# Kernel tuning notes

Measured on AMD Instinct MI355X. Metric: run time of the kernel, lower is better.

Reference implementation:

```python
import jax, jax.numpy as jnp
import numpy as np

D = 1024      # hidden_dim
E = 8         # num_experts
F = 512       # expert_dim


def setup_inputs() -> dict:
    key = jax.random.key(0)
    ks = jax.random.split(key, 7)
    B, N = 4, 4096
    s1 = 1.0 / np.sqrt(D)
    s2 = 1.0 / np.sqrt(F)
    return {
        "x": jax.random.normal(ks[0], (B, N, D), dtype=jnp.float32),
        "W1": jax.random.uniform(ks[1], (E, D, F), jnp.float32, -s1, s1),  # per-expert first linear
        "b1": jax.random.uniform(ks[2], (E, F), jnp.float32, -s1, s1),
        "W2": jax.random.uniform(ks[3], (E, F, D), jnp.float32, -s2, s2),  # per-expert second linear
        "b2": jax.random.uniform(ks[4], (E, D), jnp.float32, -s2, s2),
        "Wr": jax.random.uniform(ks[5], (D, E), jnp.float32, -s1, s1),    # router
        "br": jax.random.uniform(ks[6], (E,), jnp.float32, -s1, s1),
    }


def reference(x, W1, b1, W2, b2, Wr, br):
    # Router: softmax over experts per token. [B,N,E]
    router_weights = jax.nn.softmax(x @ Wr + br, axis=-1)
    # All experts on all tokens (dense soft-MoE), batched as grouped GEMMs.
    h = jax.nn.gelu(jnp.einsum('bnd,edf->bnef', x, W1) + b1, approximate=False)  # [B,N,E,F]
    y = jnp.einsum('bnef,efd->bned', h, W2) + b2[None, None]                      # [B,N,E,D]
    # Softmax-weighted combine over experts.
    return jnp.einsum('bned,bne->bnd', y, router_weights)
```

## Files before the change

kernel.cpp:

```cpp
#include <hip/hip_runtime.h>
#include <hip/hip_bf16.h>
#include <math.h>

#define MTOK 16384
#define DDIM 1024
#define EEXP 8
#define FDIM 512
#define EFK  4096

typedef __attribute__((ext_vector_type(8))) short short8;
typedef __attribute__((ext_vector_type(4))) float floatx4;

__device__ __forceinline__ void gld_lds16(const void* g, void* l) {
  __builtin_amdgcn_global_load_lds((const __attribute__((address_space(1))) void*)g,
                                   (__attribute__((address_space(3))) void*)l, 16, 0, 0);
}

__device__ __forceinline__ float gelu_fast(float v) {
  const float z  = v * 0.70710678118654752f;
  const float az = fabsf(z);
  const float t  = __builtin_amdgcn_rcpf(1.f + 0.3275911f * az);
  const float poly = t * (0.254829592f +
                     t * (-0.284496736f +
                     t * (1.421413741f +
                     t * (-1.453152027f +
                     t * 1.061405429f))));
  const float ex = __expf(-az * az);
  float erfv = 1.f - poly * ex;
  erfv = copysignf(erfv, z);
  return 0.5f * v * (1.f + erfv);
}

__global__ __launch_bounds__(256) void transpose_cast_kernel(
    const float* __restrict__ in, __hip_bfloat16* __restrict__ out, int R, int C) {
  __shared__ float tile[32][33];
  const float* inb = in + (size_t)blockIdx.z * R * C;
  __hip_bfloat16* outb = out + (size_t)blockIdx.z * R * C;
  const int c0 = blockIdx.x * 32, r0 = blockIdx.y * 32;
  const int tx = threadIdx.x & 31, ty = threadIdx.x >> 5;
#pragma unroll
  for (int i = 0; i < 4; ++i)
    tile[ty + i * 8][tx] = inb[(size_t)(r0 + ty + i * 8) * C + (c0 + tx)];
  __syncthreads();
#pragma unroll
  for (int i = 0; i < 4; ++i)
    outb[(size_t)(c0 + ty + i * 8) * R + (r0 + tx)] = __float2bfloat16(tile[tx][ty + i * 8]);
}

__global__ __launch_bounds__(256) void router_cast_kernel(
    const float* __restrict__ x, const float* __restrict__ Wr, const float* __restrict__ br,
    __hip_bfloat16* __restrict__ xbf, float* __restrict__ r) {
  const int wave = (blockIdx.x * 256 + threadIdx.x) >> 6;
  const int lane = threadIdx.x & 63;
  const float* xr = x + (size_t)wave * DDIM;
  float acc[EEXP];
#pragma unroll
  for (int e = 0; e < EEXP; ++e) acc[e] = 0.f;
#pragma unroll
  for (int i = 0; i < DDIM / 64; ++i) {
    const int d = i * 64 + lane;
    const float xv = xr[d];
    xbf[(size_t)wave * DDIM + d] = __float2bfloat16(xv);
    const float4* w4 = (const float4*)(Wr + (size_t)d * EEXP);
    const float4 w0 = w4[0], w1 = w4[1];
    acc[0] += xv * w0.x; acc[1] += xv * w0.y; acc[2] += xv * w0.z; acc[3] += xv * w0.w;
    acc[4] += xv * w1.x; acc[5] += xv * w1.y; acc[6] += xv * w1.z; acc[7] += xv * w1.w;
  }
#pragma unroll
  for (int off = 32; off; off >>= 1) {
#pragma unroll
    for (int e = 0; e < EEXP; ++e) acc[e] += __shfl_xor(acc[e], off, 64);
  }
  float mx = -1e30f;
#pragma unroll
  for (int e = 0; e < EEXP; ++e) { acc[e] += br[e]; mx = fmaxf(mx, acc[e]); }
  float s = 0.f;
#pragma unroll
  for (int e = 0; e < EEXP; ++e) { acc[e] = expf(acc[e] - mx); s += acc[e]; }
  const float inv = 1.f / s;
  if (lane < EEXP) r[(size_t)wave * EEXP + lane] = acc[lane] * inv;
}

#define BUFB  24576
#define BOFFB 8192

#define STAGE3(O2, K0)                                                          \
  do {                                                                          \
    gld_lds16(pA  + (K0), ldsb + (O2) + (tid << 4));                            \
    gld_lds16(pB0 + (K0), ldsb + (O2) + 8192  + (tid << 4));                    \
    gld_lds16(pB1 + (K0), ldsb + (O2) + 16384 + (tid << 4));                    \
  } while (0)

#define READS8(O0)                                                              \
  _Pragma("unroll") for (int i_ = 0; i_ < 4; ++i_)                              \
    af[i_] = *(const short8*)(ldsb + (O0) + laneA + i_ * 1024);                 \
  _Pragma("unroll") for (int j_ = 0; j_ < 4; ++j_)                              \
    bf[j_] = *(const short8*)(ldsb + (O0) + laneB + j_ * 1024);

#define MFMA16                                                                  \
  _Pragma("unroll") for (int i_ = 0; i_ < 4; ++i_)                              \
    _Pragma("unroll") for (int j_ = 0; j_ < 4; ++j_)                            \
      acc[i_][j_] = __builtin_amdgcn_mfma_f32_16x16x32_bf16(                    \
          af[i_], bf[j_], acc[i_][j_], 0, 0, 0);

#define GEMM_CORE(NT)                                                           \
  STAGE3(0, 0);                                                                 \
  STAGE3(BUFB, 32);                                                             \
  asm volatile("s_waitcnt vmcnt(3)\n\ts_barrier" ::: "memory");                 \
  {                                                                             \
    int o0 = 0, o1 = BUFB, o2 = 2 * BUFB;                                       \
    for (int kt = 0; kt < (NT) - 2; ++kt) {                                     \
      READS8(o0);                                                               \
      STAGE3(o2, (kt + 2) * 32);                                                \
      __builtin_amdgcn_s_setprio(1);                                            \
      MFMA16;                                                                   \
      __builtin_amdgcn_s_setprio(0);                                            \
      __builtin_amdgcn_sched_barrier(0);                                        \
      asm volatile("s_waitcnt vmcnt(3)\n\ts_barrier" ::: "memory");             \
      const int t_ = o0; o0 = o1; o1 = o2; o2 = t_;                             \
    }                                                                           \
    READS8(o0);                                                                 \
    __builtin_amdgcn_s_setprio(1);                                              \
    MFMA16;                                                                     \
    __builtin_amdgcn_s_setprio(0);                                              \
    __builtin_amdgcn_sched_barrier(0);                                          \
    asm volatile("s_waitcnt vmcnt(0)\n\ts_barrier" ::: "memory");               \
    READS8(o1);                                                                 \
    __builtin_amdgcn_s_setprio(1);                                              \
    MFMA16;                                                                     \
    __builtin_amdgcn_s_setprio(0);                                              \
  }

#define STAGE_PTR(gbase, LD, posv)                                              \
  ((gbase) + (size_t)(2 * ((posv) >> 3) + ((((posv) & 7) ^ (((posv) >> 3) & 7)) >> 2)) * (LD) \
           + ((((posv) & 7) ^ (((posv) >> 3) & 7)) & 3) * 8)

__global__ __launch_bounds__(512, 4) void gemm_h_kernel(
    const __hip_bfloat16* __restrict__ A, const __hip_bfloat16* __restrict__ W1t,
    const float* __restrict__ b1, const float* __restrict__ r,
    __hip_bfloat16* __restrict__ Hs) {
  const int bid = blockIdx.x;
  const int xcd = bid & 7, t = bid >> 3;
  const int strip = (t >> 5) * 8 + xcd;
  const int em = t & 31, e = em >> 2, mb = em & 3;
  const int T0 = strip * 256, F0 = mb * 128;

  __shared__ char ldsb[3 * BUFB];

  const int tid = threadIdx.x, lane = tid & 63, wid = tid >> 6;
  const int wr = wid >> 2, wc = wid & 3;
  const int lanem = lane & 15, laneq = lane >> 4;
  const int cswz = (((lanem & 1) << 2) | laneq) ^ (lanem >> 1);
  const int laneA = (lanem >> 1) * 128 + cswz * 16 + wr * 4096;
  const int laneB = BOFFB + (lanem >> 1) * 128 + cswz * 16 + wc * 4096;

  const __hip_bfloat16* gA = W1t + (size_t)e * FDIM * DDIM + (size_t)F0 * DDIM;
  const __hip_bfloat16* gB = A + (size_t)T0 * DDIM;
  const __hip_bfloat16* pA  = STAGE_PTR(gA, DDIM, tid);
  const __hip_bfloat16* pB0 = STAGE_PTR(gB, DDIM, tid);
  const __hip_bfloat16* pB1 = STAGE_PTR(gB, DDIM, tid + 512);

  floatx4 acc[4][4];
#pragma unroll
  for (int i = 0; i < 4; ++i)
#pragma unroll
    for (int j = 0; j < 4; ++j) acc[i][j] = (floatx4){0.f, 0.f, 0.f, 0.f};
  short8 af[4], bf[4];

  GEMM_CORE(DDIM / 32);

#pragma unroll
  for (int nj = 0; nj < 4; ++nj) {
    const int tok = T0 + wc * 64 + nj * 16 + lanem;
    const float rv = r[(size_t)tok * EEXP + e];
#pragma unroll
    for (int mi = 0; mi < 4; ++mi) {
      const int f = F0 + wr * 64 + mi * 16 + laneq * 4;
      const float4 b4 = *(const float4*)(b1 + e * FDIM + f);
      union { ushort4 u; __hip_bfloat16 h[4]; } pk;
      pk.h[0] = __float2bfloat16(gelu_fast(acc[mi][nj][0] + b4.x) * rv);
      pk.h[1] = __float2bfloat16(gelu_fast(acc[mi][nj][1] + b4.y) * rv);
      pk.h[2] = __float2bfloat16(gelu_fast(acc[mi][nj][2] + b4.z) * rv);
      pk.h[3] = __float2bfloat16(gelu_fast(acc[mi][nj][3] + b4.w) * rv);
      *(ushort4*)(Hs + (size_t)tok * EFK + e * FDIM + f) = pk.u;
    }
  }
}

__global__ __launch_bounds__(512, 4) void gemm_out_kernel(
    const __hip_bfloat16* __restrict__ Hs, const __hip_bfloat16* __restrict__ W2t,
    const float* __restrict__ b2, const float* __restrict__ r,
    float* __restrict__ out) {
  const int bid = blockIdx.x;
  const int xcd = bid & 7, t = bid >> 3;
  const int strip = (t >> 3) * 8 + xcd;
  const int mb = t & 7;
  const int T0 = strip * 256, D0 = mb * 128;

  __shared__ char ldsb[3 * BUFB];

  const int tid = threadIdx.x, lane = tid & 63, wid = tid >> 6;
  const int wr = wid >> 2, wc = wid & 3;
  const int lanem = lane & 15, laneq = lane >> 4;
  const int cswz = (((lanem & 1) << 2) | laneq) ^ (lanem >> 1);
  const int laneA = (lanem >> 1) * 128 + cswz * 16 + wr * 4096;
  const int laneB = BOFFB + (lanem >> 1) * 128 + cswz * 16 + wc * 4096;

  const __hip_bfloat16* gA = W2t + (size_t)D0 * EFK;
  const __hip_bfloat16* gB = Hs + (size_t)T0 * EFK;
  const __hip_bfloat16* pA  = STAGE_PTR(gA, EFK, tid);
  const __hip_bfloat16* pB0 = STAGE_PTR(gB, EFK, tid);
  const __hip_bfloat16* pB1 = STAGE_PTR(gB, EFK, tid + 512);

  floatx4 acc[4][4];
#pragma unroll
  for (int i = 0; i < 4; ++i)
#pragma unroll
    for (int j = 0; j < 4; ++j) acc[i][j] = (floatx4){0.f, 0.f, 0.f, 0.f};
  short8 af[4], bf[4];

  GEMM_CORE(EFK / 32);

#pragma unroll
  for (int mi = 0; mi < 4; ++mi) {
    const int d0 = D0 + wr * 64 + mi * 16 + laneq * 4;
    float4 b2v[EEXP];
#pragma unroll
    for (int e = 0; e < EEXP; ++e) b2v[e] = *(const float4*)(b2 + e * DDIM + d0);
#pragma unroll
    for (int nj = 0; nj < 4; ++nj) {
      const int tok = T0 + wc * 64 + nj * 16 + lanem;
      const float4* r4 = (const float4*)(r + (size_t)tok * EEXP);
      const float4 r0 = r4[0], r1 = r4[1];
      const float rv[EEXP] = {r0.x, r0.y, r0.z, r0.w, r1.x, r1.y, r1.z, r1.w};
      float bx = 0.f, by = 0.f, bz = 0.f, bw = 0.f;
#pragma unroll
      for (int e = 0; e < EEXP; ++e) {
        bx += rv[e] * b2v[e].x; by += rv[e] * b2v[e].y;
        bz += rv[e] * b2v[e].z; bw += rv[e] * b2v[e].w;
      }
      float4 o;
      o.x = acc[mi][nj][0] + bx; o.y = acc[mi][nj][1] + by;
      o.z = acc[mi][nj][2] + bz; o.w = acc[mi][nj][3] + bw;
      *(float4*)(out + (size_t)tok * DDIM + d0) = o;
    }
  }
}

extern "C" void kernel_launch(void* const* d_in, const int* in_sizes, int n_in,
                              void* d_out, int out_size, void* d_ws, size_t ws_size,
                              hipStream_t stream) {
  const float* x  = (const float*)d_in[0];
  const float* W1 = (const float*)d_in[1];
  const float* b1 = (const float*)d_in[2];
  const float* W2 = (const float*)d_in[3];
  const float* b2 = (const float*)d_in[4];
  const float* Wr = (const float*)d_in[5];
  const float* br = (const float*)d_in[6];
  float* out = (float*)d_out;

  char* ws = (char*)d_ws;
  __hip_bfloat16* xbf = (__hip_bfloat16*)(ws);
  __hip_bfloat16* W1t = (__hip_bfloat16*)(ws + (32u << 20));
  __hip_bfloat16* W2t = (__hip_bfloat16*)(ws + (40u << 20));
  float*          r   = (float*)(ws + (48u << 20));
  __hip_bfloat16* Hs  = (__hip_bfloat16*)(ws + (48u << 20) + (1u << 19));

  transpose_cast_kernel<<<dim3(FDIM / 32, DDIM / 32, EEXP), 256, 0, stream>>>(W1, W1t, DDIM, FDIM);
  transpose_cast_kernel<<<dim3(DDIM / 32, EFK / 32, 1), 256, 0, stream>>>(W2, W2t, EFK, DDIM);
  router_cast_kernel<<<MTOK / 4, 256, 0, stream>>>(x, Wr, br, xbf, r);
  gemm_h_kernel<<<dim3((MTOK / 256) * (FDIM / 128) * EEXP), 512, 0, stream>>>(xbf, W1t, b1, r, Hs);
  gemm_out_kernel<<<dim3((MTOK / 256) * (DDIM / 128)), 512, 0, stream>>>(Hs, W2t, b2, r, out);
}
```

Before: 512.6 us.

## Rework GEMM tiling to 128x128 tiles with double buffering and redesign router

Shrinks both GEMM blocks from 512 threads with 256x128 tiles to 256 threads with 128x128 tiles. The triple-buffered pipeline with manual waitcnt, setprio and sched_barrier is replaced by a simpler double-buffered loop that synchronises with __syncthreads. The router now reads a pre-transposed Wr produced by a new small kernel, casts x with vectorised float4 loads, and computes each token-expert logit in its own lane. Smaller tiles raise the block count and occupancy, but they lower operand reuse and drop the hand-tuned overlap of loads with MFMA work.

```diff
diff --git a/kernel.cpp b/kernel.cpp
--- a/kernel.cpp
+++ b/kernel.cpp
@@ -47,118 +47,106 @@
     outb[(size_t)(c0 + ty + i * 8) * R + (r0 + tx)] = __float2bfloat16(tile[tx][ty + i * 8]);
 }
 
+__global__ __launch_bounds__(256) void wrt_kernel(
+    const float* __restrict__ Wr, float* __restrict__ WrT) {
+  const int i = blockIdx.x * 256 + threadIdx.x;
+  const int d = i >> 3, e = i & 7;
+  WrT[(size_t)e * DDIM + d] = Wr[(size_t)d * EEXP + e];
+}
+
 __global__ __launch_bounds__(256) void router_cast_kernel(
-    const float* __restrict__ x, const float* __restrict__ Wr, const float* __restrict__ br,
-    __hip_bfloat16* __restrict__ xbf, float* __restrict__ r) {
-  const int wave = (blockIdx.x * 256 + threadIdx.x) >> 6;
-  const int lane = threadIdx.x & 63;
-  const float* xr = x + (size_t)wave * DDIM;
-  float acc[EEXP];
-#pragma unroll
-  for (int e = 0; e < EEXP; ++e) acc[e] = 0.f;
-#pragma unroll
-  for (int i = 0; i < DDIM / 64; ++i) {
-    const int d = i * 64 + lane;
-    const float xv = xr[d];
-    xbf[(size_t)wave * DDIM + d] = __float2bfloat16(xv);
-    const float4* w4 = (const float4*)(Wr + (size_t)d * EEXP);
-    const float4 w0 = w4[0], w1 = w4[1];
-    acc[0] += xv * w0.x; acc[1] += xv * w0.y; acc[2] += xv * w0.z; acc[3] += xv * w0.w;
-    acc[4] += xv * w1.x; acc[5] += xv * w1.y; acc[6] += xv * w1.z; acc[7] += xv * w1.w;
-  }
-#pragma unroll
-  for (int off = 32; off; off >>= 1) {
-#pragma unroll
-    for (int e = 0; e < EEXP; ++e) acc[e] += __shfl_xor(acc[e], off, 64);
-  }
-  float mx = -1e30f;
-#pragma unroll
-  for (int e = 0; e < EEXP; ++e) { acc[e] += br[e]; mx = fmaxf(mx, acc[e]); }
-  float s = 0.f;
-#pragma unroll
-  for (int e = 0; e < EEXP; ++e) { acc[e] = expf(acc[e] - mx); s += acc[e]; }
-  const float inv = 1.f / s;
-  if (lane < EEXP) r[(size_t)wave * EEXP + lane] = acc[lane] * inv;
-}
-
-#define BUFB  24576
-#define BOFFB 8192
-
-#define STAGE3(O2, K0)                                                          \
-  do {                                                                          \
-    gld_lds16(pA  + (K0), ldsb + (O2) + (tid << 4));                            \
-    gld_lds16(pB0 + (K0), ldsb + (O2) + 8192  + (tid << 4));                    \
-    gld_lds16(pB1 + (K0), ldsb + (O2) + 16384 + (tid << 4));                    \
-  } while (0)
-
-#define READS8(O0)                                                              \
-  _Pragma("unroll") for (int i_ = 0; i_ < 4; ++i_)                              \
-    af[i_] = *(const short8*)(ldsb + (O0) + laneA + i_ * 1024);                 \
-  _Pragma("unroll") for (int j_ = 0; j_ < 4; ++j_)                              \
-    bf[j_] = *(const short8*)(ldsb + (O0) + laneB + j_ * 1024);
-
-#define MFMA16                                                                  \
-  _Pragma("unroll") for (int i_ = 0; i_ < 4; ++i_)                              \
-    _Pragma("unroll") for (int j_ = 0; j_ < 4; ++j_)                            \
-      acc[i_][j_] = __builtin_amdgcn_mfma_f32_16x16x32_bf16(                    \
-          af[i_], bf[j_], acc[i_][j_], 0, 0, 0);
-
-#define GEMM_CORE(NT)                                                           \
-  STAGE3(0, 0);                                                                 \
-  STAGE3(BUFB, 32);                                                             \
-  asm volatile("s_waitcnt vmcnt(3)\n\ts_barrier" ::: "memory");                 \
-  {                                                                             \
-    int o0 = 0, o1 = BUFB, o2 = 2 * BUFB;                                       \
-    for (int kt = 0; kt < (NT) - 2; ++kt) {                                     \
-      READS8(o0);                                                               \
-      STAGE3(o2, (kt + 2) * 32);                                                \
-      __builtin_amdgcn_s_setprio(1);                                            \
-      MFMA16;                                                                   \
-      __builtin_amdgcn_s_setprio(0);                                            \
-      __builtin_amdgcn_sched_barrier(0);                                        \
-      asm volatile("s_waitcnt vmcnt(3)\n\ts_barrier" ::: "memory");             \
-      const int t_ = o0; o0 = o1; o1 = o2; o2 = t_;                             \
-    }                                                                           \
-    READS8(o0);                                                                 \
-    __builtin_amdgcn_s_setprio(1);                                              \
-    MFMA16;                                                                     \
-    __builtin_amdgcn_s_setprio(0);                                              \
-    __builtin_amdgcn_sched_barrier(0);                                          \
-    asm volatile("s_waitcnt vmcnt(0)\n\ts_barrier" ::: "memory");               \
-    READS8(o1);                                                                 \
-    __builtin_amdgcn_s_setprio(1);                                              \
-    MFMA16;                                                                     \
-    __builtin_amdgcn_s_setprio(0);                                              \
-  }
+    const float* __restrict__ x, const float* __restrict__ WrT,
+    const float* __restrict__ br, __hip_bfloat16* __restrict__ xbf,
+    float* __restrict__ r) {
+  const int wid = threadIdx.x >> 6, lane = threadIdx.x & 63;
+  const int tok0 = blockIdx.x * 32 + wid * 8;
+  const int tg = lane >> 3, e = lane & 7;
+
+  const float* xw = x + (size_t)tok0 * DDIM;
+  __hip_bfloat16* xo = xbf + (size_t)tok0 * DDIM;
+#pragma unroll 4
+  for (int it = 0; it < 32; ++it) {
+    const int o = it * 256 + lane * 4;
+    const float4 v = *(const float4*)(xw + o);
+    union { ushort4 u; __hip_bfloat16 h[4]; } pk;
+    pk.h[0] = __float2bfloat16(v.x); pk.h[1] = __float2bfloat16(v.y);
+    pk.h[2] = __float2bfloat16(v.z); pk.h[3] = __float2bfloat16(v.w);
+    *(ushort4*)(xo + o) = pk.u;
+  }
+
+  const float* xt = x + (size_t)(tok0 + tg) * DDIM;
+  const float* we = WrT + (size_t)e * DDIM;
+  float acc = 0.f;
+#pragma unroll 4
+  for (int d = 0; d < DDIM; d += 4) {
+    const float4 xv = *(const float4*)(xt + d);
+    const float4 wv = *(const float4*)(we + d);
+    acc += xv.x * wv.x + xv.y * wv.y + xv.z * wv.z + xv.w * wv.w;
+  }
+  const float logit = acc + br[e];
+  float mx = logit;
+#pragma unroll
+  for (int m = 1; m < 8; m <<= 1) mx = fmaxf(mx, __shfl_xor(mx, m));
+  const float ex = __expf(logit - mx);
+  float s = ex;
+#pragma unroll
+  for (int m = 1; m < 8; m <<= 1) s += __shfl_xor(s, m);
+  r[(size_t)(tok0 + tg) * EEXP + e] = ex / s;
+}
 
 #define STAGE_PTR(gbase, LD, posv)                                              \
   ((gbase) + (size_t)(2 * ((posv) >> 3) + ((((posv) & 7) ^ (((posv) >> 3) & 7)) >> 2)) * (LD) \
            + ((((posv) & 7) ^ (((posv) >> 3) & 7)) & 3) * 8)
 
-__global__ __launch_bounds__(512, 4) void gemm_h_kernel(
+#define STAGE4(O, K0)                                                           \
+  do {                                                                          \
+    gld_lds16(pA0 + (K0), ldsb + (O) + (tid << 4));                             \
+    gld_lds16(pA1 + (K0), ldsb + (O) + 4096 + (tid << 4));                      \
+    gld_lds16(pB0 + (K0), ldsb + (O) + 8192 + (tid << 4));                      \
+    gld_lds16(pB1 + (K0), ldsb + (O) + 12288 + (tid << 4));                     \
+  } while (0)
+
+#define GEMM_CORE(NT)                                                           \
+  STAGE4(0, 0);                                                                 \
+  for (int kt = 0; kt < (NT); ++kt) {                                           \
+    __syncthreads();                                                            \
+    const int bo = (kt & 1) << 14;                                              \
+    if (kt + 1 < (NT)) STAGE4(bo ^ 16384, (kt + 1) * 32);                       \
+    _Pragma("unroll") for (int i_ = 0; i_ < 4; ++i_)                            \
+      af[i_] = *(const short8*)(ldsb + bo + laneA + i_ * 1024);                 \
+    _Pragma("unroll") for (int j_ = 0; j_ < 4; ++j_)                            \
+      bf[j_] = *(const short8*)(ldsb + bo + laneB + j_ * 1024);                 \
+    _Pragma("unroll") for (int i_ = 0; i_ < 4; ++i_)                            \
+      _Pragma("unroll") for (int j_ = 0; j_ < 4; ++j_)                          \
+        acc[i_][j_] = __builtin_amdgcn_mfma_f32_16x16x32_bf16(                  \
+            af[i_], bf[j_], acc[i_][j_], 0, 0, 0);                              \
+  }
+
+__global__ __launch_bounds__(256, 3) void gemm_h_kernel(
     const __hip_bfloat16* __restrict__ A, const __hip_bfloat16* __restrict__ W1t,
     const float* __restrict__ b1, const float* __restrict__ r,
     __hip_bfloat16* __restrict__ Hs) {
   const int bid = blockIdx.x;
-  const int xcd = bid & 7, t = bid >> 3;
-  const int strip = (t >> 5) * 8 + xcd;
-  const int em = t & 31, e = em >> 2, mb = em & 3;
-  const int T0 = strip * 256, F0 = mb * 128;
-
-  __shared__ char ldsb[3 * BUFB];
+  const int strip = (bid >> 8) * 8 + (bid & 7);
+  const int wsl = (bid >> 3) & 31;
+  const int e = wsl >> 2, fb = wsl & 3;
+  const int T0 = strip * 128, F0 = fb * 128;
+
+  __shared__ char ldsb[2 * 16384];
 
   const int tid = threadIdx.x, lane = tid & 63, wid = tid >> 6;
-  const int wr = wid >> 2, wc = wid & 3;
+  const int wr = wid >> 1, wc = wid & 1;
   const int lanem = lane & 15, laneq = lane >> 4;
   const int cswz = (((lanem & 1) << 2) | laneq) ^ (lanem >> 1);
   const int laneA = (lanem >> 1) * 128 + cswz * 16 + wr * 4096;
-  const int laneB = BOFFB + (lanem >> 1) * 128 + cswz * 16 + wc * 4096;
+  const int laneB = 8192 + (lanem >> 1) * 128 + cswz * 16 + wc * 4096;
 
   const __hip_bfloat16* gA = W1t + (size_t)e * FDIM * DDIM + (size_t)F0 * DDIM;
   const __hip_bfloat16* gB = A + (size_t)T0 * DDIM;
-  const __hip_bfloat16* pA  = STAGE_PTR(gA, DDIM, tid);
+  const __hip_bfloat16* pA0 = STAGE_PTR(gA, DDIM, tid);
+  const __hip_bfloat16* pA1 = STAGE_PTR(gA, DDIM, tid + 256);
   const __hip_bfloat16* pB0 = STAGE_PTR(gB, DDIM, tid);
-  const __hip_bfloat16* pB1 = STAGE_PTR(gB, DDIM, tid + 512);
+  const __hip_bfloat16* pB1 = STAGE_PTR(gB, DDIM, tid + 256);
 
   floatx4 acc[4][4];
 #pragma unroll
@@ -187,30 +175,30 @@
   }
 }
 
-__global__ __launch_bounds__(512, 4) void gemm_out_kernel(
+__global__ __launch_bounds__(256, 3) void gemm_out_kernel(
     const __hip_bfloat16* __restrict__ Hs, const __hip_bfloat16* __restrict__ W2t,
     const float* __restrict__ b2, const float* __restrict__ r,
     float* __restrict__ out) {
   const int bid = blockIdx.x;
-  const int xcd = bid & 7, t = bid >> 3;
-  const int strip = (t >> 3) * 8 + xcd;
-  const int mb = t & 7;
-  const int T0 = strip * 256, D0 = mb * 128;
-
-  __shared__ char ldsb[3 * BUFB];
+  const int strip = (bid >> 6) * 8 + (bid & 7);
+  const int db = (bid >> 3) & 7;
+  const int T0 = strip * 128, D0 = db * 128;
+
+  __shared__ char ldsb[2 * 16384];
 
   const int tid = threadIdx.x, lane = tid & 63, wid = tid >> 6;
-  const int wr = wid >> 2, wc = wid & 3;
+  const int wr = wid >> 1, wc = wid & 1;
   const int lanem = lane & 15, laneq = lane >> 4;
   const int cswz = (((lanem & 1) << 2) | laneq) ^ (lanem >> 1);
   const int laneA = (lanem >> 1) * 128 + cswz * 16 + wr * 4096;
-  const int laneB = BOFFB + (lanem >> 1) * 128 + cswz * 16 + wc * 4096;
+  const int laneB = 8192 + (lanem >> 1) * 128 + cswz * 16 + wc * 4096;
 
   const __hip_bfloat16* gA = W2t + (size_t)D0 * EFK;
   const __hip_bfloat16* gB = Hs + (size_t)T0 * EFK;
-  const __hip_bfloat16* pA  = STAGE_PTR(gA, EFK, tid);
+  const __hip_bfloat16* pA0 = STAGE_PTR(gA, EFK, tid);
+  const __hip_bfloat16* pA1 = STAGE_PTR(gA, EFK, tid + 256);
   const __hip_bfloat16* pB0 = STAGE_PTR(gB, EFK, tid);
-  const __hip_bfloat16* pB1 = STAGE_PTR(gB, EFK, tid + 512);
+  const __hip_bfloat16* pB1 = STAGE_PTR(gB, EFK, tid + 256);
 
   floatx4 acc[4][4];
 #pragma unroll
@@ -265,10 +253,12 @@
   __hip_bfloat16* W2t = (__hip_bfloat16*)(ws + (40u << 20));
   float*          r   = (float*)(ws + (48u << 20));
   __hip_bfloat16* Hs  = (__hip_bfloat16*)(ws + (48u << 20) + (1u << 19));
-
+  float*          WrT = (float*)(ws + (176u << 20) + (1u << 19));
+
+  wrt_kernel<<<32, 256, 0, stream>>>(Wr, WrT);
   transpose_cast_kernel<<<dim3(FDIM / 32, DDIM / 32, EEXP), 256, 0, stream>>>(W1, W1t, DDIM, FDIM);
   transpose_cast_kernel<<<dim3(DDIM / 32, EFK / 32, 1), 256, 0, stream>>>(W2, W2t, EFK, DDIM);
-  router_cast_kernel<<<MTOK / 4, 256, 0, stream>>>(x, Wr, br, xbf, r);
-  gemm_h_kernel<<<dim3((MTOK / 256) * (FDIM / 128) * EEXP), 512, 0, stream>>>(xbf, W1t, b1, r, Hs);
-  gemm_out_kernel<<<dim3((MTOK / 256) * (DDIM / 128)), 512, 0, stream>>>(Hs, W2t, b2, r, out);
-}
+  router_cast_kernel<<<MTOK / 32, 256, 0, stream>>>(x, WrT, br, xbf, r);
+  gemm_h_kernel<<<dim3((MTOK / 128) * (FDIM / 128) * EEXP), 256, 0, stream>>>(xbf, W1t, b1, r, Hs);
+  gemm_out_kernel<<<dim3((MTOK / 128) * (DDIM / 128)), 256, 0, stream>>>(Hs, W2t, b2, r, out);
+}
```

Result: slower. 662.0 us (+29.2%).
